# Optimization experiments

Hardware: AMD Instinct MI355X
Metric: run time of the kernel (lower is better)

Reference implementation:

```python
import jax, jax.numpy as jnp
import numpy as np

B, N, D = 4, 1024, 1024
T_ITER = 4
E_TYPES = 4  # edge_type_num; module loops over E_TYPES+1 with bitmask
ALPHA = 0.2


def _lin_w(key, out_f, in_f):
    # fan-avg uniform init from custom Linear
    bound = float(np.sqrt(3.0 / ((in_f + out_f) / 2.0)))
    return jax.random.uniform(key, (out_f, in_f), minval=-bound, maxval=bound, dtype=jnp.float32)


def setup_inputs() -> dict:
    key = jax.random.key(0)
    ks = jax.random.split(key, 32)
    inp = {}
    inp['ents'] = jax.random.normal(ks[0], (B, N, D), jnp.float32)
    inp['ent_mask'] = jnp.ones((B, N), jnp.float32)
    inp['q_encoding'] = jax.random.normal(ks[1], (B, D), jnp.float32)
    inp['adj'] = jax.random.randint(ks[2], (B, N, N), 0, E_TYPES + 1, dtype=jnp.int32)
    inp['types'] = 30  # bits 1..4 set -> edge types 1..4 active
    inp['init_mem'] = jax.random.normal(ks[3], (1, D), jnp.float32)
    inp['w_qin'] = _lin_w(ks[4], D, D); inp['b_qin'] = jnp.zeros((D,), jnp.float32)
    inp['w_qt'] = jnp.stack([_lin_w(ks[5 + t], D, D) for t in range(T_ITER)])
    inp['b_qt'] = jnp.zeros((T_ITER, D), jnp.float32)
    inp['w_pl'] = _lin_w(ks[9], D, D);  inp['b_pl'] = jnp.zeros((D,), jnp.float32)
    inp['w_pc'] = _lin_w(ks[10], D, D); inp['b_pc'] = jnp.zeros((D,), jnp.float32)
    inp['w_q'] = _lin_w(ks[11], D, 3 * D); inp['b_q'] = jnp.zeros((D,), jnp.float32)
    inp['w_k'] = _lin_w(ks[12], D, 3 * D); inp['b_k'] = jnp.zeros((D,), jnp.float32)
    inp['w_v'] = _lin_w(ks[13], D, 3 * D); inp['b_v'] = jnp.zeros((D,), jnp.float32)
    inp['w_pk'] = _lin_w(ks[14], D, D); inp['b_pk'] = jnp.zeros((D,), jnp.float32)
    inp['w_pv'] = _lin_w(ks[15], D, D); inp['b_pv'] = jnp.zeros((D,), jnp.float32)
    # wes: xavier_uniform(gain=1.414) on shape (2D, 1); stored flat as (E_TYPES, 2D)
    wb = 1.414 * float(np.sqrt(6.0 / (2 * D + 1)))
    inp['wes'] = jax.random.uniform(ks[16], (E_TYPES, 2 * D), minval=-wb, maxval=wb, dtype=jnp.float32)
    inp['w_mu'] = _lin_w(ks[17], D, 2 * D); inp['b_mu'] = jnp.zeros((D,), jnp.float32)
    inp['w_cb'] = _lin_w(ks[18], D, 2 * D); inp['b_cb'] = jnp.zeros((D,), jnp.float32)
    return inp


def _lin(x, w, b):
    return x @ w.T + b


def _qdgat_forward(ents, ent_mask, q_encoding, adj, types, init_mem,
                   w_qin, b_qin, w_qt, b_qt, w_pl, b_pl, w_pc, b_pc,
                   w_q, b_q, w_k, b_k, w_v, b_v, w_pk, b_pk, w_pv, b_pv,
                   wes, w_mu, b_mu, w_cb, b_cb):
    d = ents.shape[-1]
    x_loc = ents
    x_ctx = jnp.broadcast_to(init_mem, ents.shape)
    # eval mode: var-drop mask is ones scaled by ent_mask
    var_drop = ent_mask[:, :, None]
    adj_pos = adj > 0
    q_base = jax.nn.elu(_lin(q_encoding, w_qin, b_qin))
    n_types = wes.shape[0] + 1  # self.edge_type_num = edge_type_num + 1
    for t in range(T_ITER):
        cmd = _lin(q_base, w_qt[t], b_qt[t])                      # [B,D]
        xc = x_ctx * var_drop
        pl = _lin(x_loc, w_pl, b_pl)
        pc = _lin(xc, w_pc, b_pc)
        x_joint = jnp.concatenate([x_loc, xc, pl * pc], axis=-1)   # [B,N,3D]
        q = _lin(x_joint, w_q, b_q)                               # [B,N,D]
        k = _lin(x_joint, w_k, b_k) * _lin(cmd, w_pk, b_pk)[:, None, :]
        v = _lin(x_joint, w_v, b_v) * _lin(cmd, w_pv, b_pv)[:, None, :]
        # edge_score[b,i,j] = sum over active types T of (adj==T) * (q_i . we[:D] + k_j . we[D:])
        # equivalent to matmul((cat(q_i,k_j) * (adj==T)), we) without materializing [B,N,N,2D]
        edge_score = jnp.zeros(adj.shape, jnp.float32)
        for i in range(n_types):
            if (types >> i) & 1 == 1:
                w1, w2 = wes[i - 1, :d], wes[i - 1, d:]  # i=0 aliases wes[-1], as in torch
                s = (q @ w1)[:, :, None] + (k @ w2)[:, None, :]    # [B,N,N]
                edge_score = edge_score + jnp.where(adj == i, s, 0.0)
        e = jnp.where(edge_score > 0, edge_score, ALPHA * edge_score)  # leaky relu
        logits = jnp.where(adj_pos, e, jnp.float32(-9e15))
        prob = jax.nn.softmax(logits, axis=-1)                     # [B,N,N]
        message = jnp.einsum('bij,bjd->bid', prob, v)
        x_ctx = _lin(jnp.concatenate([xc, message], axis=-1), w_mu, b_mu)
    return _lin(jnp.concatenate([x_loc, x_ctx], axis=-1), w_cb, b_cb)


def reference(ents, ent_mask, q_encoding, adj, types, init_mem,
              w_qin, b_qin, w_qt, b_qt, w_pl, b_pl, w_pc, b_pc,
              w_q, b_q, w_k, b_k, w_v, b_v, w_pk, b_pk, w_pv, b_pv,
              wes, w_mu, b_mu, w_cb, b_cb):
    return _qdgat_forward(ents, ent_mask, q_encoding, adj, types, init_mem,
                          w_qin, b_qin, w_qt, b_qt, w_pl, b_pl, w_pc, b_pc,
                          w_q, b_q, w_k, b_k, w_v, b_v, w_pk, b_pk, w_pv, b_pv,
                          wes, w_mu, b_mu, w_cb, b_cb)
```

## Files before the change

kernel.cpp:

```cpp
#include <hip/hip_runtime.h>
#include <hip/hip_bf16.h>
#include <stdint.h>
#include <stddef.h>


typedef __hip_bfloat16 bf16;
typedef __attribute__((ext_vector_type(8))) short short8;
typedef __attribute__((ext_vector_type(4))) float floatx4;

#define NB 4
#define NN 1024
#define DD 1024
#define NT_ITER 4
#define MM (NB * NN)

static __device__ __forceinline__ float b2f(bf16 x) { return __bfloat162float(x); }
static __device__ __forceinline__ bf16 f2b(float x) { return __float2bfloat16(x); }
static __device__ __forceinline__ unsigned short f2bu(float x) {
    bf16 h = __float2bfloat16(x);
    unsigned short u;
    __builtin_memcpy(&u, &h, 2);
    return u;
}
static __device__ __forceinline__ float bu2f(unsigned short u) {
    unsigned int t = (unsigned int)u << 16;
    float f;
    __builtin_memcpy(&f, &t, 4);
    return f;
}

static __device__ __forceinline__ void gl_lds16(const void* g, void* l) {
    __builtin_amdgcn_global_load_lds(
        (const __attribute__((address_space(1))) unsigned int*)g,
        (__attribute__((address_space(3))) unsigned int*)l, 16, 0, 0);
}

template <int N>
static __device__ __forceinline__ void s_wait_vmcnt() {
    if constexpr (N == 0)      asm volatile("s_waitcnt vmcnt(0)" ::: "memory");
    else if constexpr (N == 4) asm volatile("s_waitcnt vmcnt(4)" ::: "memory");
    else if constexpr (N == 6) asm volatile("s_waitcnt vmcnt(6)" ::: "memory");
    else if constexpr (N == 8) asm volatile("s_waitcnt vmcnt(8)" ::: "memory");
}

__global__ void k_f2b(const float* __restrict__ src, bf16* __restrict__ dst, int n4) {
    int i = blockIdx.x * 256 + threadIdx.x;
    if (i >= n4) return;
    float4 v = ((const float4*)src)[i];
    ushort4 o;
    o.x = f2bu(v.x); o.y = f2bu(v.y); o.z = f2bu(v.z); o.w = f2bu(v.w);
    ((ushort4*)dst)[i] = o;
}

__global__ void k_transw(const float* __restrict__ src, bf16* __restrict__ dst) {
    __shared__ float tile[32][33];
    int c0 = blockIdx.x * 32;
    int r0 = blockIdx.y * 32;
    int tx = threadIdx.x, ty = threadIdx.y;
    for (int i = 0; i < 32; i += 8)
        tile[ty + i][tx] = src[(size_t)(r0 + ty + i) * 3072 + c0 + tx];
    __syncthreads();
    for (int i = 0; i < 32; i += 8)
        dst[(size_t)(c0 + ty + i) * 1024 + r0 + tx] = f2b(tile[tx][ty + i]);
}

__global__ void k_build_sc(const float* __restrict__ pk, const float* __restrict__ wes,
                           bf16* __restrict__ Aq, bf16* __restrict__ Ak) {
    int i = blockIdx.x * 256 + threadIdx.x;
    int half = i >> 16;
    int j = i & 65535;
    int row = j >> 10, d = j & 1023;
    if (half == 0) {
        Aq[j] = (row < 4) ? f2b(wes[(size_t)row * 2048 + d]) : f2b(0.f);
    } else {
        int t = row >> 4, b = (row >> 2) & 3, e = row & 3;
        Ak[j] = f2b(pk[((size_t)t * NB + b) * DD + d] * wes[(size_t)e * 2048 + 1024 + d]);
    }
}

__global__ __launch_bounds__(256) void k_qbase(const float* __restrict__ qenc, const float* __restrict__ w,
                                               const float* __restrict__ b, float* __restrict__ out) {
    int o = blockIdx.x * 4 + (threadIdx.x >> 6);
    int lane = threadIdx.x & 63;
    int n = o >> 2, r = o & 3;
    const float* xr = qenc + (size_t)r * DD;
    const float* wr = w + (size_t)n * DD;
    float s = 0.f;
    for (int d = lane; d < DD; d += 64) s += xr[d] * wr[d];
    for (int off = 32; off; off >>= 1) s += __shfl_down(s, off);
    if (lane == 0) {
        s += b[n];
        out[(size_t)r * DD + n] = s > 0.f ? s : (expf(s) - 1.0f);
    }
}

__global__ __launch_bounds__(256) void k_cmd(const float* __restrict__ qb, const float* __restrict__ w_qt,
                                             const float* __restrict__ b_qt, float* __restrict__ cmd) {
    int o = blockIdx.x * 4 + (threadIdx.x >> 6);
    int lane = threadIdx.x & 63;
    int r = o & 3, n = (o >> 2) & 1023, t = o >> 12;
    const float* xr = qb + (size_t)r * DD;
    const float* wr = w_qt + ((size_t)t * DD + n) * DD;
    float s = 0.f;
    for (int d = lane; d < DD; d += 64) s += xr[d] * wr[d];
    for (int off = 32; off; off >>= 1) s += __shfl_down(s, off);
    if (lane == 0) cmd[((size_t)t * NB + r) * DD + n] = s + b_qt[t * DD + n];
}

__global__ __launch_bounds__(256) void k_pkpv(const float* __restrict__ cmd,
                                              const float* __restrict__ w_pk, const float* __restrict__ b_pk,
                                              const float* __restrict__ w_pv, const float* __restrict__ b_pv,
                                              float* __restrict__ pk, float* __restrict__ pv) {
    int o = blockIdx.x * 4 + (threadIdx.x >> 6);
    int lane = threadIdx.x & 63;
    int n = o >> 5, half = (o >> 4) & 1, pair = o & 15;
    const float* xr = cmd + (size_t)pair * DD;
    const float* wr = (half ? w_pv : w_pk) + (size_t)n * DD;
    float s = 0.f;
    for (int d = lane; d < DD; d += 64) s += xr[d] * wr[d];
    for (int off = 32; off; off >>= 1) s += __shfl_down(s, off);
    if (lane == 0)
        (half ? pv : pk)[(size_t)pair * DD + n] = s + (half ? b_pv : b_pk)[n];
}

__global__ void k_consts(const float* __restrict__ b_q, const float* __restrict__ b_k,
                         const float* __restrict__ pk, const float* __restrict__ wes,
                         float* __restrict__ cq, float* __restrict__ ck) {
    int o = blockIdx.x;
    int lane = threadIdx.x;
    float s = 0.f;
    if (o < 4) {
        for (int d = lane; d < 1024; d += 64) s += b_q[d] * wes[(size_t)o * 2048 + d];
    } else {
        int oo = o - 4;
        int t = oo >> 4, b = (oo >> 2) & 3, e = oo & 3;
        for (int d = lane; d < 1024; d += 64)
            s += b_k[d] * pk[((size_t)t * NB + b) * DD + d] * wes[(size_t)e * 2048 + 1024 + d];
    }
    for (int off = 32; off; off >>= 1) s += __shfl_down(s, off);
    if (lane == 0) {
        if (o < 4) cq[o] = s;
        else ck[o - 4] = s;
    }
}

__global__ __launch_bounds__(256) void k_qakb2(const bf16* __restrict__ ents, const bf16* __restrict__ xc,
                                               const bf16* __restrict__ plpc,
                                               const float* __restrict__ wqtw, const float* __restrict__ wkeff_t,
                                               const float* __restrict__ cq, const float* __restrict__ ck_t,
                                               float* __restrict__ qa, float* __restrict__ kb) {
    __shared__ float red[4][8];
    int m = blockIdx.x;
    int b = m >> 10;
    int t = threadIdx.x;
    float aq[4] = {0.f, 0.f, 0.f, 0.f}, ak[4] = {0.f, 0.f, 0.f, 0.f};
    const bf16* rows[3] = {ents + (size_t)m * DD, xc + (size_t)m * DD, plpc + (size_t)m * DD};
#pragma unroll
    for (int c = 0; c < 3; ++c) {
        ushort4 rv = *(const ushort4*)(rows[c] + 4 * t);
        float xv0 = bu2f(rv.x), xv1 = bu2f(rv.y), xv2 = bu2f(rv.z), xv3 = bu2f(rv.w);
        const float* wq = wqtw + c * 1024 + 4 * t;
        const float* wk = wkeff_t + (size_t)b * 4 * 3072 + c * 1024 + 4 * t;
#pragma unroll
        for (int e = 0; e < 4; ++e) {
            float4 q4 = *(const float4*)(wq + (size_t)e * 3072);
            float4 k4 = *(const float4*)(wk + (size_t)e * 3072);
            aq[e] += xv0 * q4.x + xv1 * q4.y + xv2 * q4.z + xv3 * q4.w;
            ak[e] += xv0 * k4.x + xv1 * k4.y + xv2 * k4.z + xv3 * k4.w;
        }
    }
#pragma unroll
    for (int e = 0; e < 4; ++e) {
        float v = aq[e];
        for (int o = 32; o; o >>= 1) v += __shfl_down(v, o);
        if ((t & 63) == 0) red[t >> 6][e] = v;
        v = ak[e];
        for (int o = 32; o; o >>= 1) v += __shfl_down(v, o);
        if ((t & 63) == 0) red[t >> 6][e + 4] = v;
    }
    __syncthreads();
    if (t < 8) {
        float s = red[0][t] + red[1][t] + red[2][t] + red[3][t];
        if (t < 4) qa[(size_t)m * 4 + t] = s + cq[t];
        else kb[(size_t)m * 4 + (t - 4)] = s + ck_t[b * 4 + (t - 4)];
    }
}

__global__ void k_init(const bf16* __restrict__ initm_bf, const float* __restrict__ mask,
                       bf16* __restrict__ x_ctx, bf16* __restrict__ xc) {
    int i = blockIdx.x * 256 + threadIdx.x;
    uint4 v = ((const uint4*)initm_bf)[i & 127];
    ((uint4*)x_ctx)[i] = v;
    float mk = mask[i >> 7];
    unsigned short* u = (unsigned short*)&v;
#pragma unroll
    for (int j = 0; j < 8; ++j) u[j] = f2bu(bu2f(u[j]) * mk);
    ((uint4*)xc)[i] = v;
}

template <int WM, int WN>
__device__ __forceinline__ void gemm_core(
    const bf16* __restrict__ A0, const bf16* __restrict__ A1, const bf16* __restrict__ A2,
    const bf16* __restrict__ W, const float* __restrict__ bias, void* __restrict__ C,
    const void* __restrict__ mul, const float* __restrict__ addC, bf16* __restrict__ C2,
    int mulmode, int storef32, int nchunks, int ldw, int ldc,
    int bm, int bn) {
    constexpr int BM = WM * 2;
    constexpr int BN = WN * 2;
    constexpr int MI = WM / 16;
    constexpr int NI = WN / 16;
    constexpr int SEGS = (BM + BN) / 8;
    constexpr int SPW = SEGS / 4;
    __shared__ bf16 sAB[3][(BM + BN) * 64];

    const int t = threadIdx.x;
    const int lane = t & 63;
    const int w = t >> 6;
    const int wm = (w & 1) * WM, wn = (w >> 1) * WN;
    const int srow = lane >> 3;
    const int scol = ((lane & 7) * 8) ^ (srow << 3);

    floatx4 acc[MI][NI];
#pragma unroll
    for (int i = 0; i < MI; ++i)
#pragma unroll
        for (int j = 0; j < NI; ++j) acc[i][j] = (floatx4){0.f, 0.f, 0.f, 0.f};

    const int lrow = lane & 15;
    const int kq = (lane >> 4) * 8;
    const int kx = (lane & 7) << 3;
    const int ktiles = nchunks * 16;

    auto stage = [&](int buf, int kt) {
        const int cidx = kt >> 4;
        const bf16* Ac = (cidx == 0) ? A0 : (cidx == 1 ? A1 : A2);
        const int klocal = (kt & 15) * 64;
        const int kglob = kt * 64;
#pragma unroll
        for (int s = 0; s < SPW; ++s) {
            int c = w * SPW + s;
            if (c < BM / 8) {
                const bf16* src = Ac + ((size_t)(bm * BM + c * 8 + srow)) * 1024 + klocal + scol;
                gl_lds16(src, &sAB[buf][c * 512]);
            } else {
                const bf16* src = W + ((size_t)(bn * BN + (c - BM / 8) * 8 + srow)) * (size_t)ldw + kglob + scol;
                gl_lds16(src, &sAB[buf][c * 512]);
            }
        }
    };

    stage(0, 0);
    if (ktiles > 1) stage(1, 1);
    int cur = 0, sb = 2;
    for (int kt = 0; kt < ktiles; ++kt) {
        if (kt + 1 < ktiles) s_wait_vmcnt<SPW>();
        else s_wait_vmcnt<0>();
        __builtin_amdgcn_s_barrier();
        __builtin_amdgcn_sched_barrier(0);
        short8 af[2][MI], bfr[2][NI];
#pragma unroll
        for (int ks = 0; ks < 2; ++ks) {
            const int ko = (ks * 32 + kq) ^ kx;
#pragma unroll
            for (int mi = 0; mi < MI; ++mi)
                af[ks][mi] = *(const short8*)&sAB[cur][(wm + mi * 16 + lrow) * 64 + ko];
#pragma unroll
            for (int ni = 0; ni < NI; ++ni)
                bfr[ks][ni] = *(const short8*)&sAB[cur][BM * 64 + (wn + ni * 16 + lrow) * 64 + ko];
        }
        if (kt + 2 < ktiles) stage(sb, kt + 2);
        __builtin_amdgcn_s_setprio(1);
#pragma unroll
        for (int ks = 0; ks < 2; ++ks)
#pragma unroll
            for (int mi = 0; mi < MI; ++mi)
#pragma unroll
                for (int ni = 0; ni < NI; ++ni)
                    acc[mi][ni] = __builtin_amdgcn_mfma_f32_16x16x32_bf16(af[ks][mi], bfr[ks][ni], acc[mi][ni], 0, 0, 0);
        __builtin_amdgcn_s_setprio(0);
        asm volatile("s_waitcnt lgkmcnt(0)" ::: "memory");
        __builtin_amdgcn_sched_barrier(0);
        cur = (cur == 2) ? 0 : cur + 1;
        sb = (sb == 2) ? 0 : sb + 1;
    }

    const int qrow = (lane >> 4) * 4;
#pragma unroll
    for (int mi = 0; mi < MI; ++mi) {
#pragma unroll
        for (int ni = 0; ni < NI; ++ni) {
            int gn = bn * BN + wn + ni * 16 + lrow;
            float bv = bias ? bias[gn] : 0.f;
#pragma unroll
            for (int r = 0; r < 4; ++r) {
                int gm = bm * BM + wm + mi * 16 + qrow + r;
                size_t ci = (size_t)gm * (size_t)ldc + gn;
                float val = acc[mi][ni][r] + bv;
                if (addC) val += addC[ci];
                if (mulmode == 1)
                    val *= b2f(((const bf16*)mul)[(size_t)gm * 1024 + gn]);
                else if (mulmode == 2)
                    val *= ((const float*)mul)[(size_t)(gm >> 10) * 1024 + gn];
                if (storef32) {
                    ((float*)C)[ci] = val;
                } else {
                    ((bf16*)C)[ci] = f2b(val);
                    if (mulmode == 3)
                        C2[ci] = f2b(val * ((const float*)mul)[gm]);
                }
            }
        }
    }
}

template <int WM, int WN>
__global__ __launch_bounds__(256) void k_gemm_t(
    const bf16* __restrict__ A0, const bf16* __restrict__ A1, const bf16* __restrict__ A2,
    const bf16* __restrict__ W, const float* __restrict__ bias, void* __restrict__ C,
    const void* __restrict__ mul, const float* __restrict__ addC, bf16* __restrict__ C2,
    int mulmode, int storef32, int nchunks, int ldw, int ldc,
    long long sA, long long sW, long long sC) {
    int bz = blockIdx.z;
    const bf16* A0b = A0 + (size_t)bz * sA;
    const bf16* Wb = W + (size_t)bz * sW;
    void* Cb = storef32 ? (void*)((float*)C + (size_t)bz * sC)
                        : (void*)((bf16*)C + (size_t)bz * sC);
    int gx = gridDim.x, gy = gridDim.y;
    int nwg = gx * gy;
    int bx, by;
    if ((nwg & 7) == 0) {
        int o = blockIdx.y * gx + blockIdx.x;
        int q = nwg >> 3;
        int lid = (o & 7) * q + (o >> 3);
        bx = lid % gx;
        by = lid / gx;
    } else {
        bx = blockIdx.x;
        by = blockIdx.y;
    }
    gemm_core<WM, WN>(A0b, A1, A2, Wb, bias, Cb, mul, addC, C2, mulmode, storef32, nchunks, ldw, ldc,
                      bx, by);
}

__global__ void k_transpose(const bf16* __restrict__ v, bf16* __restrict__ vT) {
    __shared__ bf16 tile[32][33];
    int b = blockIdx.z;
    int n0 = blockIdx.x * 32, d0 = blockIdx.y * 32;
    int tx = threadIdx.x, ty = threadIdx.y;
    for (int i = 0; i < 32; i += 8)
        tile[ty + i][tx] = v[((size_t)b * NN + n0 + ty + i) * DD + d0 + tx];
    __syncthreads();
    for (int i = 0; i < 32; i += 8)
        vT[((size_t)b * DD + d0 + ty + i) * NN + n0 + tx] = tile[tx][ty + i];
}

__global__ __launch_bounds__(256) void k_attn(const int* __restrict__ adj, const float* __restrict__ qa,
                                              const float* __restrict__ kb, const int* __restrict__ typesPtr,
                                              bf16* __restrict__ prob) {
    __shared__ float lg[NN];
    __shared__ float red[4];
    __shared__ float red2[4];
    int m = blockIdx.x;
    int b = m >> 10;
    int t = threadIdx.x;
    int types = typesPtr[0];
    float qa4[4];
#pragma unroll
    for (int e = 0; e < 4; ++e) qa4[e] = qa[(size_t)m * 4 + e];
    const int* arow = adj + (size_t)m * NN;
    const float* kbb = kb + (size_t)(b << 10) * 4;

    float lmax = -3.0e38f;
    for (int j = t; j < NN; j += 256) {
        int a = arow[j];
        float l;
        if (a == 0) {
            l = -9.0e15f;
        } else if ((types >> a) & 1) {
            float s = qa4[a - 1] + kbb[(size_t)j * 4 + (a - 1)];
            l = s > 0.f ? s : 0.2f * s;
        } else {
            l = 0.f;
        }
        lg[j] = l;
        lmax = fmaxf(lmax, l);
    }
    for (int o = 32; o > 0; o >>= 1) lmax = fmaxf(lmax, __shfl_down(lmax, o));
    if ((t & 63) == 0) red[t >> 6] = lmax;
    __syncthreads();
    lmax = fmaxf(fmaxf(red[0], red[1]), fmaxf(red[2], red[3]));

    float lsum = 0.f;
    for (int j = t; j < NN; j += 256) {
        float ex = __expf(lg[j] - lmax);
        lg[j] = ex;
        lsum += ex;
    }
    for (int o = 32; o > 0; o >>= 1) lsum += __shfl_down(lsum, o);
    if ((t & 63) == 0) red2[t >> 6] = lsum;
    __syncthreads();
    lsum = red2[0] + red2[1] + red2[2] + red2[3];
    float inv = 1.0f / lsum;

    bf16* prow = prob + (size_t)m * NN;
    for (int j = t; j < NN; j += 256) prow[j] = f2b(lg[j] * inv);
}

extern "C" void kernel_launch(void* const* d_in, const int* in_sizes, int n_in,
                              void* d_out, int out_size, void* d_ws, size_t ws_size,
                              hipStream_t stream) {
    const float* ents = (const float*)d_in[0];
    const float* mask = (const float*)d_in[1];
    const float* qenc = (const float*)d_in[2];
    const int* adj = (const int*)d_in[3];
    const int* types = (const int*)d_in[4];
    const float* initm = (const float*)d_in[5];
    const float* w_qin = (const float*)d_in[6];
    const float* b_qin = (const float*)d_in[7];
    const float* w_qt = (const float*)d_in[8];
    const float* b_qt = (const float*)d_in[9];
    const float* w_pl = (const float*)d_in[10];
    const float* b_pl = (const float*)d_in[11];
    const float* w_pc = (const float*)d_in[12];
    const float* b_pc = (const float*)d_in[13];
    const float* w_q = (const float*)d_in[14];
    const float* b_q = (const float*)d_in[15];
    const float* w_k = (const float*)d_in[16];
    const float* b_k = (const float*)d_in[17];
    const float* w_v = (const float*)d_in[18];
    const float* b_v = (const float*)d_in[19];
    const float* w_pk = (const float*)d_in[20];
    const float* b_pk = (const float*)d_in[21];
    const float* w_pv = (const float*)d_in[22];
    const float* b_pv = (const float*)d_in[23];
    const float* wes = (const float*)d_in[24];
    const float* w_mu = (const float*)d_in[25];
    const float* b_mu = (const float*)d_in[26];
    const float* w_cb = (const float*)d_in[27];
    const float* b_cb = (const float*)d_in[28];
    (void)in_sizes; (void)n_in; (void)out_size; (void)ws_size;

    char* p = (char*)d_ws;
    auto carve = [&](size_t bytes) {
        char* r = p;
        p += (bytes + 255) & ~(size_t)255;
        return r;
    };
    float* q_base = (float*)carve((size_t)NB * DD * 4);
    float* cmd = (float*)carve((size_t)NT_ITER * NB * DD * 4);
    float* pk = (float*)carve((size_t)NT_ITER * NB * DD * 4);
    float* pv = (float*)carve((size_t)NT_ITER * NB * DD * 4);
    float* qa = (float*)carve((size_t)MM * 4 * 4);
    float* kb = (float*)carve((size_t)MM * 4 * 4);
    float* wqtw = (float*)carve((size_t)64 * 3072 * 4);
    float* wkeff = (float*)carve((size_t)64 * 3072 * 4);
    float* cq = (float*)carve(4 * 4);
    float* ck = (float*)carve(64 * 4);
    float* vent = (float*)carve((size_t)MM * DD * 4);
    bf16* initm_bf = (bf16*)carve((size_t)DD * 2);
    bf16* ents_bf = (bf16*)carve((size_t)MM * DD * 2);
    bf16* wpl_bf = (bf16*)carve((size_t)DD * DD * 2);
    bf16* wpc_bf = (bf16*)carve((size_t)DD * DD * 2);
    bf16* wv_bf = (bf16*)carve((size_t)DD * 3 * DD * 2);
    bf16* wmu_bf = (bf16*)carve((size_t)DD * 2 * DD * 2);
    bf16* wcb_bf = (bf16*)carve((size_t)DD * 2 * DD * 2);
    bf16* wqT_bf = (bf16*)carve((size_t)3 * DD * DD * 2);
    bf16* wkT_bf = (bf16*)carve((size_t)3 * DD * DD * 2);
    bf16* Aq = (bf16*)carve((size_t)64 * DD * 2);
    bf16* Ak = (bf16*)carve((size_t)64 * DD * 2);
    bf16* x_ctx = (bf16*)carve((size_t)MM * DD * 2);
    bf16* xc = (bf16*)carve((size_t)MM * DD * 2);
    bf16* pl = (bf16*)carve((size_t)MM * DD * 2);
    bf16* plpc = (bf16*)carve((size_t)MM * DD * 2);
    bf16* vbuf = (bf16*)carve((size_t)MM * DD * 2);
    bf16* msg = (bf16*)carve((size_t)MM * DD * 2);
    bf16* prob = (bf16*)carve((size_t)NB * NN * NN * 2);
    bf16* vT = plpc;

    const dim3 blk(256);
    const dim3 g128(32, 16, 1);
    const dim3 gMsg(8, 16, NB);
    const dim3 gPre(1, 48, 1);

    k_f2b<<<1, blk, 0, stream>>>(initm, initm_bf, DD / 4);
    k_f2b<<<4096, blk, 0, stream>>>(ents, ents_bf, MM * DD / 4);
    k_f2b<<<1024, blk, 0, stream>>>(w_pl, wpl_bf, DD * DD / 4);
    k_f2b<<<1024, blk, 0, stream>>>(w_pc, wpc_bf, DD * DD / 4);
    k_f2b<<<3072, blk, 0, stream>>>(w_v, wv_bf, DD * 3 * DD / 4);
    k_f2b<<<2048, blk, 0, stream>>>(w_mu, wmu_bf, DD * 2 * DD / 4);
    k_f2b<<<2048, blk, 0, stream>>>(w_cb, wcb_bf, DD * 2 * DD / 4);
    k_transw<<<dim3(96, 32), dim3(32, 8), 0, stream>>>(w_q, wqT_bf);
    k_transw<<<dim3(96, 32), dim3(32, 8), 0, stream>>>(w_k, wkT_bf);

    k_qbase<<<1024, blk, 0, stream>>>(qenc, w_qin, b_qin, q_base);
    k_cmd<<<4096, blk, 0, stream>>>(q_base, w_qt, b_qt, cmd);
    k_pkpv<<<8192, blk, 0, stream>>>(cmd, w_pk, b_pk, w_pv, b_pv, pk, pv);
    k_init<<<2048, blk, 0, stream>>>(initm_bf, mask, x_ctx, xc);

    k_build_sc<<<512, blk, 0, stream>>>(pk, wes, Aq, Ak);
    k_consts<<<68, 64, 0, stream>>>(b_q, b_k, pk, wes, cq, ck);
    k_gemm_t<32, 32><<<gPre, blk, 0, stream>>>(Aq, nullptr, nullptr, wqT_bf, nullptr, wqtw,
                                               nullptr, nullptr, nullptr, 0, 1, 1, 1024, 3072, 0, 0, 0);
    k_gemm_t<32, 32><<<gPre, blk, 0, stream>>>(Ak, nullptr, nullptr, wkT_bf, nullptr, wkeff,
                                               nullptr, nullptr, nullptr, 0, 1, 1, 1024, 3072, 0, 0, 0);

    k_gemm_t<64, 32><<<g128, blk, 0, stream>>>(ents_bf, nullptr, nullptr, wpl_bf, b_pl, pl,
                                               nullptr, nullptr, nullptr, 0, 0, 1, 1024, 1024, 0, 0, 0);
    k_gemm_t<64, 32><<<g128, blk, 0, stream>>>(ents_bf, nullptr, nullptr, wv_bf, nullptr, vent,
                                               nullptr, nullptr, nullptr, 0, 1, 1, 3072, 1024, 0, 0, 0);

    for (int t = 0; t < NT_ITER; ++t) {
        k_gemm_t<64, 32><<<g128, blk, 0, stream>>>(xc, nullptr, nullptr, wpc_bf, b_pc, plpc,
                                                   pl, nullptr, nullptr, 1, 0, 1, 1024, 1024, 0, 0, 0);
        k_gemm_t<64, 32><<<g128, blk, 0, stream>>>(xc, plpc, nullptr, wv_bf + 1024, b_v, vbuf,
                                                   pv + (size_t)t * NB * DD, vent, nullptr, 2, 0, 2, 3072, 1024, 0, 0, 0);
        k_qakb2<<<4096, blk, 0, stream>>>(ents_bf, xc, plpc,
                                          wqtw, wkeff + (size_t)t * 16 * 3072,
                                          cq, ck + t * 16, qa, kb);
        k_transpose<<<dim3(32, 32, NB), dim3(32, 8), 0, stream>>>(vbuf, vT);
        k_attn<<<4096, blk, 0, stream>>>(adj, qa, kb, types, prob);
        k_gemm_t<64, 32><<<gMsg, blk, 0, stream>>>(prob, nullptr, nullptr, vT, nullptr, msg,
                                                   nullptr, nullptr, nullptr, 0, 0, 1, 1024, 1024,
                                                   (long long)NN * NN, (long long)DD * NN, (long long)NN * DD);
        k_gemm_t<64, 32><<<g128, blk, 0, stream>>>(xc, msg, nullptr, wmu_bf, b_mu, x_ctx,
                                                   mask, nullptr, xc, 3, 0, 2, 2048, 1024, 0, 0, 0);
    }
    k_gemm_t<64, 32><<<g128, blk, 0, stream>>>(ents_bf, x_ctx, nullptr, wcb_bf, b_cb, (float*)d_out,
                                               nullptr, nullptr, nullptr, 0, 1, 2, 2048, 1024, 0, 0, 0);
}
```

Before: 988.9 us.

## Precompute byte-coded adjacency once and register-resident vectorized attention softmax

```diff
diff --git a/kernel.cpp b/kernel.cpp
--- a/kernel.cpp
+++ b/kernel.cpp
@@ -62,6 +62,21 @@
     __syncthreads();
     for (int i = 0; i < 32; i += 8)
         dst[(size_t)(c0 + ty + i) * 1024 + r0 + tx] = f2b(tile[tx][ty + i]);
+}
+
+__global__ void k_adjcode(const int* __restrict__ adj, const int* __restrict__ typesPtr,
+                          unsigned char* __restrict__ code, int n4) {
+    int i = blockIdx.x * 256 + threadIdx.x;
+    if (i >= n4) return;
+    int types = typesPtr[0];
+    int4 a4 = ((const int4*)adj)[i];
+    uchar4 c;
+    int a;
+    a = a4.x; c.x = (a == 0) ? 255 : (((types >> a) & 1) ? (unsigned char)(a - 1) : 254);
+    a = a4.y; c.y = (a == 0) ? 255 : (((types >> a) & 1) ? (unsigned char)(a - 1) : 254);
+    a = a4.z; c.z = (a == 0) ? 255 : (((types >> a) & 1) ? (unsigned char)(a - 1) : 254);
+    a = a4.w; c.w = (a == 0) ? 255 : (((types >> a) & 1) ? (unsigned char)(a - 1) : 254);
+    ((uchar4*)code)[i] = c;
 }
 
 __global__ void k_build_sc(const float* __restrict__ pk, const float* __restrict__ wes,
@@ -325,21 +340,8 @@
     const bf16* Wb = W + (size_t)bz * sW;
     void* Cb = storef32 ? (void*)((float*)C + (size_t)bz * sC)
                         : (void*)((bf16*)C + (size_t)bz * sC);
-    int gx = gridDim.x, gy = gridDim.y;
-    int nwg = gx * gy;
-    int bx, by;
-    if ((nwg & 7) == 0) {
-        int o = blockIdx.y * gx + blockIdx.x;
-        int q = nwg >> 3;
-        int lid = (o & 7) * q + (o >> 3);
-        bx = lid % gx;
-        by = lid / gx;
-    } else {
-        bx = blockIdx.x;
-        by = blockIdx.y;
-    }
     gemm_core<WM, WN>(A0b, A1, A2, Wb, bias, Cb, mul, addC, C2, mulmode, storef32, nchunks, ldw, ldc,
-                      bx, by);
+                      blockIdx.x, blockIdx.y);
 }
 
 __global__ void k_transpose(const bf16* __restrict__ v, bf16* __restrict__ vT) {
@@ -354,56 +356,59 @@
         vT[((size_t)b * DD + d0 + ty + i) * NN + n0 + tx] = tile[tx][ty + i];
 }
 
-__global__ __launch_bounds__(256) void k_attn(const int* __restrict__ adj, const float* __restrict__ qa,
-                                              const float* __restrict__ kb, const int* __restrict__ typesPtr,
+__global__ __launch_bounds__(256) void k_attn(const unsigned char* __restrict__ code,
+                                              const float* __restrict__ qa,
+                                              const float* __restrict__ kb,
                                               bf16* __restrict__ prob) {
-    __shared__ float lg[NN];
     __shared__ float red[4];
     __shared__ float red2[4];
     int m = blockIdx.x;
     int b = m >> 10;
     int t = threadIdx.x;
-    int types = typesPtr[0];
-    float qa4[4];
-#pragma unroll
-    for (int e = 0; e < 4; ++e) qa4[e] = qa[(size_t)m * 4 + e];
-    const int* arow = adj + (size_t)m * NN;
+    float qa0 = qa[(size_t)m * 4 + 0];
+    float qa1 = qa[(size_t)m * 4 + 1];
+    float qa2 = qa[(size_t)m * 4 + 2];
+    float qa3 = qa[(size_t)m * 4 + 3];
     const float* kbb = kb + (size_t)(b << 10) * 4;
 
-    float lmax = -3.0e38f;
-    for (int j = t; j < NN; j += 256) {
-        int a = arow[j];
-        float l;
-        if (a == 0) {
-            l = -9.0e15f;
-        } else if ((types >> a) & 1) {
-            float s = qa4[a - 1] + kbb[(size_t)j * 4 + (a - 1)];
-            l = s > 0.f ? s : 0.2f * s;
-        } else {
-            l = 0.f;
+    uchar4 c4 = *(const uchar4*)(code + (size_t)m * NN + 4 * t);
+    float l0, l1, l2, l3;
+    {
+        unsigned char cc[4] = {c4.x, c4.y, c4.z, c4.w};
+        float lv[4];
+#pragma unroll
+        for (int jj = 0; jj < 4; ++jj) {
+            int j = 4 * t + jj;
+            float4 k4 = *(const float4*)(kbb + (size_t)j * 4);
+            unsigned char c = cc[jj];
+            float kv = (c == 0) ? k4.x : ((c == 1) ? k4.y : ((c == 2) ? k4.z : k4.w));
+            float qv = (c == 0) ? qa0 : ((c == 1) ? qa1 : ((c == 2) ? qa2 : qa3));
+            float s = qv + kv;
+            s = s > 0.f ? s : 0.2f * s;
+            lv[jj] = (c == 255) ? -9.0e15f : ((c == 254) ? 0.f : s);
         }
-        lg[j] = l;
-        lmax = fmaxf(lmax, l);
-    }
+        l0 = lv[0]; l1 = lv[1]; l2 = lv[2]; l3 = lv[3];
+    }
+
+    float lmax = fmaxf(fmaxf(l0, l1), fmaxf(l2, l3));
     for (int o = 32; o > 0; o >>= 1) lmax = fmaxf(lmax, __shfl_down(lmax, o));
     if ((t & 63) == 0) red[t >> 6] = lmax;
     __syncthreads();
     lmax = fmaxf(fmaxf(red[0], red[1]), fmaxf(red[2], red[3]));
 
-    float lsum = 0.f;
-    for (int j = t; j < NN; j += 256) {
-        float ex = __expf(lg[j] - lmax);
-        lg[j] = ex;
-        lsum += ex;
-    }
+    float e0 = __expf(l0 - lmax), e1 = __expf(l1 - lmax);
+    float e2 = __expf(l2 - lmax), e3 = __expf(l3 - lmax);
+    float lsum = (e0 + e1) + (e2 + e3);
     for (int o = 32; o > 0; o >>= 1) lsum += __shfl_down(lsum, o);
     if ((t & 63) == 0) red2[t >> 6] = lsum;
     __syncthreads();
     lsum = red2[0] + red2[1] + red2[2] + red2[3];
     float inv = 1.0f / lsum;
 
-    bf16* prow = prob + (size_t)m * NN;
-    for (int j = t; j < NN; j += 256) prow[j] = f2b(lg[j] * inv);
+    ushort4 o4;
+    o4.x = f2bu(e0 * inv); o4.y = f2bu(e1 * inv);
+    o4.z = f2bu(e2 * inv); o4.w = f2bu(e3 * inv);
+    ((ushort4*)(prob + (size_t)m * NN))[t] = o4;
 }
 
 extern "C" void kernel_launch(void* const* d_in, const int* in_sizes, int n_in,
@@ -468,6 +473,7 @@
     bf16* wkT_bf = (bf16*)carve((size_t)3 * DD * DD * 2);
     bf16* Aq = (bf16*)carve((size_t)64 * DD * 2);
     bf16* Ak = (bf16*)carve((size_t)64 * DD * 2);
+    unsigned char* code = (unsigned char*)carve((size_t)MM * NN);
     bf16* x_ctx = (bf16*)carve((size_t)MM * DD * 2);
     bf16* xc = (bf16*)carve((size_t)MM * DD * 2);
     bf16* pl = (bf16*)carve((size_t)MM * DD * 2);
@@ -491,6 +497,7 @@
     k_f2b<<<2048, blk, 0, stream>>>(w_cb, wcb_bf, DD * 2 * DD / 4);
     k_transw<<<dim3(96, 32), dim3(32, 8), 0, stream>>>(w_q, wqT_bf);
     k_transw<<<dim3(96, 32), dim3(32, 8), 0, stream>>>(w_k, wkT_bf);
+    k_adjcode<<<4096, blk, 0, stream>>>(adj, types, code, MM * NN / 4);
 
     k_qbase<<<1024, blk, 0, stream>>>(qenc, w_qin, b_qin, q_base);
     k_cmd<<<4096, blk, 0, stream>>>(q_base, w_qt, b_qt, cmd);
@@ -518,7 +525,7 @@
                                           wqtw, wkeff + (size_t)t * 16 * 3072,
                                           cq, ck + t * 16, qa, kb);
         k_transpose<<<dim3(32, 32, NB), dim3(32, 8), 0, stream>>>(vbuf, vT);
-        k_attn<<<4096, blk, 0, stream>>>(adj, qa, kb, types, prob);
+        k_attn<<<4096, blk, 0, stream>>>(code, qa, kb, prob);
         k_gemm_t<64, 32><<<gMsg, blk, 0, stream>>>(prob, nullptr, nullptr, vT, nullptr, msg,
                                                    nullptr, nullptr, nullptr, 0, 0, 1, 1024, 1024,
                                                    (long long)NN * NN, (long long)DD * NN, (long long)NN * DD);
```

New measurement: 940.5 us. -4.9%, faster.
